# Performance work log

Hardware: AMD Instinct MI355X
Metric: run time of the kernel (lower is better)

Reference implementation:

```python
import jax, jax.numpy as jnp
import numpy as np
import math

NUM_HEADS = 16
KEY_SIZE = 64
HIDDEN = 4096
EMBED = 1024
VOCAB = 32000
SEQ = 2048
LAYERS = 4


def rmsnorm(x):
    return x * jax.lax.rsqrt(jnp.mean(x * x, axis=-1, keepdims=True) + 1e-5)


def rope_buffers(seq, d):
    half = d // 2
    i = jnp.arange(d)
    offset = i % half
    scales = jnp.power(10000.0, (-2.0 / d) * offset.astype(jnp.float32))
    m = jnp.arange(seq, dtype=jnp.float32)
    angles = m[:, None] * scales[None, :]  # [S, D]
    cos = jnp.cos(angles)
    sin = jnp.sin(angles)
    sin = jnp.concatenate([-sin[:, :half], sin[:, half:]], axis=-1)
    return cos, sin


def rotate(x, cos, sin):
    # x: [B, H, S, D]; cos/sin: [S, D]
    half = KEY_SIZE // 2
    swapped = jnp.concatenate([x[..., half:], x[..., :half]], axis=-1)
    return cos[None, None] * x + sin[None, None] * swapped


def setup_inputs() -> dict:
    key = jax.random.key(0)
    ks = jax.random.split(key, 7)
    std = 0.02
    return {
        'tokens': jax.random.randint(ks[0], (1, SEQ), 0, VOCAB),
        'table': jax.random.normal(ks[1], (VOCAB, EMBED), jnp.float32) * std,
        'qkv_w': jax.random.normal(ks[2], (LAYERS, EMBED, 3 * NUM_HEADS * KEY_SIZE), jnp.float32) * std,
        'out_w': jax.random.normal(ks[3], (LAYERS, NUM_HEADS * KEY_SIZE, EMBED), jnp.float32) * std,
        'up_w': jax.random.normal(ks[4], (LAYERS, EMBED, 2 * HIDDEN), jnp.float32) * std,
        'down_w': jax.random.normal(ks[5], (LAYERS, HIDDEN, EMBED), jnp.float32) * std,
        'vocab_w': jax.random.normal(ks[6], (EMBED, VOCAB), jnp.float32) * std,
    }


def reference(tokens, table, qkv_w, out_w, up_w, down_w, vocab_w):
    B, S = tokens.shape
    H, D = NUM_HEADS, KEY_SIZE
    # module zeroes embedding row 0 each forward
    table = table.at[0].set(0.0)
    cos, sin = rope_buffers(S, D)
    causal = jnp.tril(jnp.ones((S, S), dtype=bool))  # context_size == S -> pure causal
    emb = table[tokens]  # [B, S, E]
    for l in range(LAYERS):
        # --- self attention ---
        normed = rmsnorm(emb)
        qkv = normed @ qkv_w[l]  # [B, S, 3HD]
        q, k, v = jnp.split(qkv, 3, axis=-1)
        q = q.reshape(B, S, H, D).transpose(0, 2, 1, 3)
        k = k.reshape(B, S, H, D).transpose(0, 2, 1, 3)
        v = v.reshape(B, S, H, D).transpose(0, 2, 1, 3)
        q = rotate(q, cos, sin)
        k = rotate(k, cos, sin)
        attn = jnp.einsum('bhqd,bhkd->bhqk', q, k) / math.sqrt(D)
        attn = jnp.where(causal[None, None], attn, -jnp.inf)
        attn = jax.nn.softmax(attn, axis=-1)
        out = jnp.einsum('bhqk,bhkd->bhqd', attn, v)
        out = out.transpose(0, 2, 1, 3).reshape(B, S, H * D)
        emb = emb + out @ out_w[l]
        # --- SwiGLU FFN ---
        normed = rmsnorm(emb)
        gate_up = normed @ up_w[l]
        gate, up = gate_up[..., :HIDDEN], gate_up[..., HIDDEN:]
        emb = emb + (up * jax.nn.silu(gate)) @ down_w[l]
    emb = rmsnorm(emb)
    logits = emb @ vocab_w  # [B, S, V]
    return logits
```

## Files before the change

kernel.cpp:

```cpp
#include <hip/hip_runtime.h>
#include <hip/hip_bf16.h>

typedef __attribute__((ext_vector_type(8))) short short8;
typedef __attribute__((ext_vector_type(4))) float f32x4;

__device__ __forceinline__ ushort f2bf(float f) {
  uint32_t u = __float_as_uint(f);
  uint32_t r = (u + 0x7FFFu + ((u >> 16) & 1u)) >> 16;
  return (ushort)r;
}
__device__ __forceinline__ float bf2f(ushort u) {
  return __uint_as_float(((uint32_t)u) << 16);
}

__device__ __forceinline__ void gload_lds16(const ushort* g, ushort* l) {
  __builtin_amdgcn_global_load_lds(
      (const __attribute__((address_space(1))) void*)g,
      (__attribute__((address_space(3))) void*)l, 16, 0, 0);
}

__device__ __forceinline__ f32x4 mfma16(short8 a, short8 b, f32x4 c) {
  return __builtin_amdgcn_mfma_f32_16x16x32_bf16(a, b, c, 0, 0, 0);
}

#define BAR() __builtin_amdgcn_s_barrier()
#define WAIT_LGKM()                                        \
  do {                                                     \
    asm volatile("s_waitcnt lgkmcnt(0)" ::: "memory");     \
    __builtin_amdgcn_sched_barrier(0);                     \
  } while (0)
#define WAIT_VM0()                                         \
  do {                                                     \
    asm volatile("s_waitcnt vmcnt(0)" ::: "memory");       \
    __builtin_amdgcn_sched_barrier(0);                     \
  } while (0)
#define WAIT_VM4()                                         \
  do {                                                     \
    asm volatile("s_waitcnt vmcnt(4)" ::: "memory");       \
    __builtin_amdgcn_sched_barrier(0);                     \
  } while (0)

__global__ __launch_bounds__(256)
void transpose_conv_kernel(const float* __restrict__ W, ushort* __restrict__ WT,
                           const int K, const int N, const int mode) {
  const size_t lofs = (size_t)blockIdx.z * K * N;
  W += lofs;
  WT += lofs;
  __shared__ float tile[64][65];
  const int n0 = blockIdx.x * 64;
  const int k0 = blockIdx.y * 64;
  const int t = threadIdx.x;
#pragma unroll
  for (int j = 0; j < 4; ++j) {
    const int idx = j * 1024 + t * 4;
    const int kk = idx >> 6, nn = idx & 63;
    *(float4*)&tile[kk][nn] = *(const float4*)&W[(size_t)(k0 + kk) * N + n0 + nn];
  }
  __syncthreads();
#pragma unroll
  for (int j = 0; j < 4; ++j) {
    const int idx = j * 1024 + t * 4;
    const int nn = idx >> 6, kk = idx & 63;
    int rr = n0 + nn;
    if (mode == 1) rr = (rr < 4096) ? (2 * rr) : (2 * (rr - 4096) + 1);
    ushort4 o;
    o.x = f2bf(tile[kk + 0][nn]);
    o.y = f2bf(tile[kk + 1][nn]);
    o.z = f2bf(tile[kk + 2][nn]);
    o.w = f2bf(tile[kk + 3][nn]);
    *(ushort4*)&WT[(size_t)rr * K + k0 + kk] = o;
  }
}

__global__ __launch_bounds__(256)
void sincos_kernel(float2* __restrict__ cstab) {
  const int idx = blockIdx.x * 256 + threadIdx.x;
  const int s = idx >> 5, o = idx & 31;
  const float freq = exp2f(-0.41524101186092029f * (float)o);
  const float a = (float)s * freq;
  cstab[idx] = make_float2(cosf(a), sinf(a));
}

__global__ __launch_bounds__(256)
void embed_norm_kernel(const int* __restrict__ tokens, const float* __restrict__ table,
                       float* __restrict__ emb, ushort* __restrict__ normed) {
  const int s = blockIdx.x, t = threadIdx.x;
  const int tok = tokens[s];
  float4 v = make_float4(0.f, 0.f, 0.f, 0.f);
  if (tok != 0) v = *(const float4*)&table[(size_t)tok * 1024 + t * 4];
  *(float4*)&emb[(size_t)s * 1024 + t * 4] = v;
  float ss = v.x * v.x + v.y * v.y + v.z * v.z + v.w * v.w;
#pragma unroll
  for (int off = 32; off; off >>= 1) ss += __shfl_xor(ss, off);
  __shared__ float red[4];
  if ((t & 63) == 0) red[t >> 6] = ss;
  __syncthreads();
  const float total = red[0] + red[1] + red[2] + red[3];
  const float sc = rsqrtf(total * (1.f / 1024.f) + 1e-5f);
  ushort4 o;
  o.x = f2bf(v.x * sc); o.y = f2bf(v.y * sc);
  o.z = f2bf(v.z * sc); o.w = f2bf(v.w * sc);
  *(ushort4*)&normed[(size_t)s * 1024 + t * 4] = o;
}

__global__ __launch_bounds__(256)
void rmsnorm_kernel(const float* __restrict__ x, ushort* __restrict__ out) {
  const int row = blockIdx.x, t = threadIdx.x;
  const float4 v = *(const float4*)&x[(size_t)row * 1024 + t * 4];
  float ss = v.x * v.x + v.y * v.y + v.z * v.z + v.w * v.w;
#pragma unroll
  for (int off = 32; off; off >>= 1) ss += __shfl_xor(ss, off);
  __shared__ float red[4];
  if ((t & 63) == 0) red[t >> 6] = ss;
  __syncthreads();
  const float total = red[0] + red[1] + red[2] + red[3];
  const float sc = rsqrtf(total * (1.f / 1024.f) + 1e-5f);
  ushort4 o;
  o.x = f2bf(v.x * sc); o.y = f2bf(v.y * sc);
  o.z = f2bf(v.z * sc); o.w = f2bf(v.w * sc);
  *(ushort4*)&out[(size_t)row * 1024 + t * 4] = o;
}

__global__ __launch_bounds__(256)
void attn_mfma_kernel(const ushort* __restrict__ qh, const ushort* __restrict__ kh,
                      const ushort* __restrict__ vt, ushort* __restrict__ attn_out) {
  __shared__ ushort sQ[64 * 64];
  __shared__ ushort sK[64 * 64];
  __shared__ ushort sV[64 * 64];
  __shared__ ushort sP[4][1024];
  const int h = blockIdx.y;
  const int bx = blockIdx.x;
  const int qt = (h < 8) ? bx : 31 - bx;
  const int i0 = qt * 64;
  const int tid = threadIdx.x;
  const int w = tid >> 6, lane = tid & 63;
  const int llo = lane & 15, lhi = lane >> 4;
  const int lr = lane >> 3, lc = lane & 7;
  const ushort* qg = qh + ((size_t)h * 2048 + i0) * 64;
  const ushort* kg = kh + (size_t)h * 2048 * 64;
  const ushort* vg = vt + (size_t)h * 64 * 2048;

#pragma unroll
  for (int j = 0; j < 2; ++j) {
    const int r0 = (w * 2 + j) * 8;
    const int row = r0 + lr;
    gload_lds16(qg + (size_t)row * 64 + ((lc ^ (row & 7)) * 8), &sQ[r0 * 64]);
  }
  __syncthreads();
  const int qrow = w * 16 + llo;
  const short8 qf0 = *(const short8*)&sQ[qrow * 64 + ((lhi ^ (qrow & 7)) * 8)];
  const short8 qf1 = *(const short8*)&sQ[qrow * 64 + (((4 + lhi) ^ (qrow & 7)) * 8)];

  float m = -1e30f, lsum = 0.f;
  f32x4 o[4] = {};
  const int nch = qt + 1;
  for (int cb = 0; cb < nch; ++cb) {
    const int kb = cb * 64;
    __syncthreads();
#pragma unroll
    for (int j = 0; j < 2; ++j) {
      const int r0 = (w * 2 + j) * 8;
      const int row = r0 + lr;
      gload_lds16(kg + (size_t)(kb + row) * 64 + ((lc ^ (row & 7)) * 8), &sK[r0 * 64]);
      gload_lds16(vg + (size_t)row * 2048 + kb + ((lc ^ (row & 7)) * 8), &sV[r0 * 64]);
    }
    __syncthreads();

    f32x4 st[4] = {};
#pragma unroll
    for (int ck = 0; ck < 2; ++ck) {
      const short8 qf = ck ? qf1 : qf0;
#pragma unroll
      for (int f = 0; f < 4; ++f) {
        const int key = f * 16 + llo;
        const short8 kf = *(const short8*)&sK[key * 64 + (((ck * 4 + lhi) ^ (key & 7)) * 8)];
        st[f] = mfma16(kf, qf, st[f]);
      }
    }

    float pv[4][4];
    const bool diag = (kb == i0);
#pragma unroll
    for (int f = 0; f < 4; ++f)
#pragma unroll
      for (int r = 0; r < 4; ++r) {
        float x = st[f][r] * 0.125f;
        if (diag && (f * 16 + lhi * 4 + r) > qrow) x = -1e30f;
        pv[f][r] = x;
      }
    float mr = pv[0][0];
#pragma unroll
    for (int f = 0; f < 4; ++f)
#pragma unroll
      for (int r = 0; r < 4; ++r) mr = fmaxf(mr, pv[f][r]);
    mr = fmaxf(mr, __shfl_xor(mr, 16));
    mr = fmaxf(mr, __shfl_xor(mr, 32));
    const float mnew = fmaxf(m, mr);
    const float scale = __expf(m - mnew);
    m = mnew;
    float rs = 0.f;
#pragma unroll
    for (int f = 0; f < 4; ++f)
#pragma unroll
      for (int r = 0; r < 4; ++r) {
        const float p = __expf(pv[f][r] - mnew);
        pv[f][r] = p;
        rs += p;
      }
    rs += __shfl_xor(rs, 16);
    rs += __shfl_xor(rs, 32);
    lsum = lsum * scale + rs;
    float scr[4];
#pragma unroll
    for (int r = 0; r < 4; ++r) scr[r] = __shfl(scale, lhi * 4 + r);
#pragma unroll
    for (int nn = 0; nn < 4; ++nn)
#pragma unroll
      for (int r = 0; r < 4; ++r) o[nn][r] *= scr[r];

    ushort* pw = sP[w];
#pragma unroll
    for (int f = 0; f < 4; ++f) {
      uint2 pk;
      pk.x = (uint)f2bf(pv[f][0]) | ((uint)f2bf(pv[f][1]) << 16);
      pk.y = (uint)f2bf(pv[f][2]) | ((uint)f2bf(pv[f][3]) << 16);
      *(uint2*)&pw[llo * 64 + ((f * 16 + lhi * 4) ^ ((llo & 7) << 3))] = pk;
    }
    const short8 pf0 = *(const short8*)&pw[llo * 64 + ((lhi ^ (llo & 7)) * 8)];
    const short8 pf1 = *(const short8*)&pw[llo * 64 + (((4 + lhi) ^ (llo & 7)) * 8)];

#pragma unroll
    for (int ck = 0; ck < 2; ++ck) {
      const short8 pf = ck ? pf1 : pf0;
#pragma unroll
      for (int nn = 0; nn < 4; ++nn) {
        const int drow = nn * 16 + llo;
        const short8 vf = *(const short8*)&sV[drow * 64 + (((ck * 4 + lhi) ^ (drow & 7)) * 8)];
        o[nn] = mfma16(pf, vf, o[nn]);
      }
    }
  }

  const float inv = 1.f / lsum;
  float invr[4];
#pragma unroll
  for (int r = 0; r < 4; ++r) invr[r] = __shfl(inv, lhi * 4 + r);
#pragma unroll
  for (int nn = 0; nn < 4; ++nn)
#pragma unroll
    for (int r = 0; r < 4; ++r) {
      const int row = i0 + w * 16 + lhi * 4 + r;
      attn_out[(size_t)row * 1024 + h * 64 + nn * 16 + llo] = f2bf(o[nn][r] * invr[r]);
    }
}

template <int BM, int BN, int EPI>
__global__ __launch_bounds__(256)
void gemm_bt64_kernel(const ushort* __restrict__ A, const ushort* __restrict__ BT,
                      const float* __restrict__ addend, void* __restrict__ Cout,
                      const int M, const int N, const int K) {
  constexpr int WM = BM / 2, WN = BN / 2;
  constexpr int FM = WM / 16, FN = WN / 16;
  __shared__ ushort sA[BM * 64];
  __shared__ ushort sB[BN * 64];
  const int bm0 = blockIdx.y * BM;
  const int bn0 = blockIdx.x * BN;
  const int tid = threadIdx.x;
  const int wid = tid >> 6, lane = tid & 63;
  const int wr = wid >> 1, wc = wid & 1;
  const int lhi = lane >> 4, llo = lane & 15;
  f32x4 acc[FM][FN] = {};
  for (int kt = 0; kt < K; kt += 64) {
#pragma unroll
    for (int i = 0; i < BM * 8 / 256; ++i) {
      const int cb = i * 256 + wid * 64;
      const int ch = cb + lane;
      const int row = ch >> 3, c = ch & 7;
      gload_lds16(A + (size_t)(bm0 + row) * K + kt + ((c ^ (row & 7)) * 8),
                  sA + (size_t)cb * 8);
    }
#pragma unroll
    for (int i = 0; i < BN * 8 / 256; ++i) {
      const int cb = i * 256 + wid * 64;
      const int ch = cb + lane;
      const int row = ch >> 3, c = ch & 7;
      gload_lds16(BT + (size_t)(bn0 + row) * K + kt + ((c ^ (row & 7)) * 8),
                  sB + (size_t)cb * 8);
    }
    __syncthreads();
    short8 aF[FM][2], bF[FN][2];
#pragma unroll
    for (int mm = 0; mm < FM; ++mm) {
      const int row = wr * WM + mm * 16 + llo;
#pragma unroll
      for (int ks = 0; ks < 2; ++ks)
        aF[mm][ks] = *(const short8*)&sA[row * 64 + (((ks * 4 + lhi) ^ (row & 7)) * 8)];
    }
#pragma unroll
    for (int nn = 0; nn < FN; ++nn) {
      const int row = wc * WN + nn * 16 + llo;
#pragma unroll
      for (int ks = 0; ks < 2; ++ks)
        bF[nn][ks] = *(const short8*)&sB[row * 64 + (((ks * 4 + lhi) ^ (row & 7)) * 8)];
    }
#pragma unroll
    for (int mm = 0; mm < FM; ++mm)
#pragma unroll
      for (int nn = 0; nn < FN; ++nn)
#pragma unroll
        for (int ks = 0; ks < 2; ++ks)
          acc[mm][nn] = mfma16(aF[mm][ks], bF[nn][ks], acc[mm][nn]);
    __syncthreads();
  }
#pragma unroll
  for (int mm = 0; mm < FM; ++mm) {
#pragma unroll
    for (int nn = 0; nn < FN; ++nn) {
      const int col = bn0 + wc * WN + nn * 16 + llo;
#pragma unroll
      for (int r = 0; r < 4; ++r) {
        const int row = bm0 + wr * WM + mm * 16 + lhi * 4 + r;
        float v = acc[mm][nn][r];
        if constexpr (EPI == 1) v += addend[(size_t)row * N + col];
        ((float*)Cout)[(size_t)row * N + col] = v;
      }
    }
  }
}

__global__ __launch_bounds__(256)
void gemm_qkv_kernel(const ushort* __restrict__ A, const ushort* __restrict__ BT,
                     const float2* __restrict__ cstab, ushort* __restrict__ qh,
                     ushort* __restrict__ kh, ushort* __restrict__ vt, const int K) {
  constexpr int BM = 128, BN = 128, WM = 64, WN = 64, FM = 4, FN = 4;
  __shared__ ushort sA[BM * 64];
  __shared__ ushort sB[BN * 64];
  const int bm0 = blockIdx.y * BM;
  const int bn0 = blockIdx.x * BN;
  const int tid = threadIdx.x;
  const int wid = tid >> 6, lane = tid & 63;
  const int wr = wid >> 1, wc = wid & 1;
  const int lhi = lane >> 4, llo = lane & 15;
  f32x4 acc[FM][FN] = {};
  for (int kt = 0; kt < K; kt += 64) {
#pragma unroll
    for (int i = 0; i < 4; ++i) {
      const int cb = i * 256 + wid * 64;
      const int ch = cb + lane;
      const int row = ch >> 3, c = ch & 7;
      gload_lds16(A + (size_t)(bm0 + row) * K + kt + ((c ^ (row & 7)) * 8),
                  sA + (size_t)cb * 8);
    }
#pragma unroll
    for (int i = 0; i < 4; ++i) {
      const int cb = i * 256 + wid * 64;
      const int ch = cb + lane;
      const int row = ch >> 3, c = ch & 7;
      gload_lds16(BT + (size_t)(bn0 + row) * K + kt + ((c ^ (row & 7)) * 8),
                  sB + (size_t)cb * 8);
    }
    __syncthreads();
    short8 aF[FM][2], bF[FN][2];
#pragma unroll
    for (int mm = 0; mm < FM; ++mm) {
      const int row = wr * WM + mm * 16 + llo;
#pragma unroll
      for (int ks = 0; ks < 2; ++ks)
        aF[mm][ks] = *(const short8*)&sA[row * 64 + (((ks * 4 + lhi) ^ (row & 7)) * 8)];
    }
#pragma unroll
    for (int nn = 0; nn < FN; ++nn) {
      const int row = wc * WN + nn * 16 + llo;
#pragma unroll
      for (int ks = 0; ks < 2; ++ks)
        bF[nn][ks] = *(const short8*)&sB[row * 64 + (((ks * 4 + lhi) ^ (row & 7)) * 8)];
    }
#pragma unroll
    for (int mm = 0; mm < FM; ++mm)
#pragma unroll
      for (int nn = 0; nn < FN; ++nn)
#pragma unroll
        for (int ks = 0; ks < 2; ++ks)
          acc[mm][nn] = mfma16(aF[mm][ks], bF[nn][ks], acc[mm][nn]);
    __syncthreads();
  }
#pragma unroll
  for (int mm = 0; mm < FM; ++mm) {
    const int row_base = bm0 + wr * WM + mm * 16 + lhi * 4;
#pragma unroll
    for (int nn = 0; nn < FN; ++nn) {
      const int col = bn0 + wc * WN + nn * 16 + llo;
      const int part = col >> 10;
      const int hcol = col & 1023;
      const int h = hcol >> 6;
      const int d = hcol & 63;
      const int off = d & 31;
      if (part == 2) {
        ushort4 o;
        o.x = f2bf(acc[mm][nn][0]);
        o.y = f2bf(acc[mm][nn][1]);
        o.z = f2bf(acc[mm][nn][2]);
        o.w = f2bf(acc[mm][nn][3]);
        *(ushort4*)&vt[((size_t)h * 64 + d) * 2048 + row_base] = o;
      } else {
#pragma unroll
        for (int r = 0; r < 4; ++r) {
          const int row = row_base + r;
          const float v = acc[mm][nn][r];
          const float pt = acc[mm][nn ^ 2][r];
          const float2 cn = cstab[row * 32 + off];
          const float si = (d < 32) ? -cn.y : cn.y;
          const ushort o = f2bf(cn.x * v + si * pt);
          const size_t ho = ((size_t)h * 2048 + row) * 64 + d;
          if (part == 0) qh[ho] = o; else kh[ho] = o;
        }
      }
    }
  }
}

#define LDA_(MH)                                                              \
  {                                                                           \
    _Pragma("unroll") for (int mm = 0; mm < 4; ++mm) {                        \
      const int row = wr * 128 + ((MH) * 4 + mm) * 16 + llo;                  \
      _Pragma("unroll") for (int ks = 0; ks < 2; ++ks)                        \
          aF[mm][ks] = *(const short8*)&cA[row * 64 +                         \
                          (((ks * 4 + lhi) ^ (row & 7)) * 8)];                \
    }                                                                         \
  }
#define LDB_(NH)                                                              \
  {                                                                           \
    _Pragma("unroll") for (int nn = 0; nn < 2; ++nn) {                        \
      const int row = wc * 64 + ((NH) * 2 + nn) * 16 + llo;                   \
      _Pragma("unroll") for (int ks = 0; ks < 2; ++ks)                        \
          bF[nn][ks] = *(const short8*)&cB[row * 64 +                         \
                          (((ks * 4 + lhi) ^ (row & 7)) * 8)];                \
    }                                                                         \
  }
#define MFMAQ_(MH, NH)                                                        \
  {                                                                           \
    __builtin_amdgcn_s_setprio(1);                                            \
    _Pragma("unroll") for (int mm = 0; mm < 4; ++mm)                          \
        _Pragma("unroll") for (int nn = 0; nn < 2; ++nn)                      \
            _Pragma("unroll") for (int ks = 0; ks < 2; ++ks)                  \
                acc[(MH) * 4 + mm][(NH) * 2 + nn] =                           \
                    mfma16(aF[mm][ks], bF[nn][ks],                            \
                           acc[(MH) * 4 + mm][(NH) * 2 + nn]);                \
    __builtin_amdgcn_s_setprio(0);                                            \
  }

template <int EPI>
__global__ __launch_bounds__(512, 2)
void gemm8_kernel(const ushort* __restrict__ A, const ushort* __restrict__ BT,
                  void* __restrict__ Cout,
                  const int M, const int N, const int K, const int nby) {
  extern __shared__ ushort smem[];
  const int nwg = gridDim.x;
  const int cpx = nwg >> 3;
  int id = blockIdx.x;
  id = (id & 7) * cpx + (id >> 3);
  const int by = id % nby, bx = id / nby;
  const int bm0 = by * 256, bn0 = bx * 256;
  const int tid = threadIdx.x;
  const int wid = tid >> 6, lane = tid & 63;
  const int wr = wid >> 2, wc = wid & 3;
  const int llo = lane & 15, lhi = lane >> 4;
  const ushort* gA = A + (size_t)bm0 * K;
  const ushort* gB = BT + (size_t)bn0 * K;

  auto stage = [&](const ushort* g, ushort* dst, int kt) {
#pragma unroll
    for (int i = 0; i < 4; ++i) {
      const int chunk = i * 512 + wid * 64 + lane;
      const int row = chunk >> 3, c = chunk & 7;
      gload_lds16(g + (size_t)row * K + kt + ((c ^ (row & 7)) * 8),
                  dst + (size_t)(i * 512 + wid * 64) * 8);
    }
  };

  f32x4 acc[8][4] = {};
  short8 aF[4][2];
  short8 bF[2][2];

  stage(gA, smem, 0);
  stage(gB, smem + 16384, 0);
  WAIT_VM0();
  BAR();

  const int nt = K >> 6;
  for (int t = 0; t < nt; ++t) {
    const int cur = t & 1;
    ushort* cA = smem + cur * 32768;
    ushort* cB = cA + 16384;
    ushort* nA = smem + (cur ^ 1) * 32768;
    ushort* nB = nA + 16384;
    const bool pf = (t + 1 < nt);
    LDA_(0); LDB_(0);
    if (pf) { stage(gA, nA, (t + 1) * 64); stage(gB, nB, (t + 1) * 64); }
    BAR(); WAIT_LGKM();
    MFMAQ_(0, 0);
    BAR();
    LDB_(1);
    BAR(); WAIT_LGKM();
    MFMAQ_(0, 1);
    BAR();
    LDA_(1);
    BAR(); WAIT_LGKM();
    MFMAQ_(1, 1);
    BAR();
    LDB_(0);
    BAR(); WAIT_LGKM();
    MFMAQ_(1, 0);
    if (pf) WAIT_VM0();
    BAR();
  }

#pragma unroll
  for (int m = 0; m < 8; ++m) {
#pragma unroll
    for (int n = 0; n < 4; ++n) {
      const int col = bn0 + wc * 64 + n * 16 + llo;
#pragma unroll
      for (int r = 0; r < 4; ++r) {
        const int row = bm0 + wr * 128 + m * 16 + lhi * 4 + r;
        float v = acc[m][n][r];
        if constexpr (EPI == 3) {
          const float other = __shfl_xor(v, 1);
          if ((llo & 1) == 0) {
            const float gate = v, up = other;
            const float hh = up * gate / (1.f + expf(-gate));
            ((ushort*)Cout)[(size_t)row * (N >> 1) + (col >> 1)] = f2bf(hh);
          }
        } else {
          ((float*)Cout)[(size_t)row * N + col] = v;
        }
      }
    }
  }
}

template <int EPI>
__global__ __launch_bounds__(512, 2)
void gemm8p_kernel(const ushort* __restrict__ A, const ushort* __restrict__ BT,
                   void* __restrict__ Cout,
                   const int M, const int N, const int K, const int nby) {
  extern __shared__ ushort smem[];
  const int nwg = gridDim.x;
  const int cpx = nwg >> 3;
  int id = blockIdx.x;
  id = (id & 7) * cpx + (id >> 3);
  const int by = id % nby, bx = id / nby;
  const int bm0 = by * 256, bn0 = bx * 256;
  const int tid = threadIdx.x;
  const int wid = tid >> 6, lane = tid & 63;
  const int wr = wid >> 2, wc = wid & 3;
  const int llo = lane & 15, lhi = lane >> 4;
  const ushort* gA = A + (size_t)bm0 * K;
  const ushort* gB = BT + (size_t)bn0 * K;

  auto stage = [&](ushort* dst, int kt) {
#pragma unroll
    for (int i = 0; i < 2; ++i) {
      const int cb = i * 512 + wid * 64;
      const int ch = cb + lane;
      const int row = ch >> 2, c = ch & 3;
      gload_lds16(gA + (size_t)row * K + kt + ((c ^ ((row >> 1) & 3)) * 8),
                  dst + (size_t)cb * 8);
    }
#pragma unroll
    for (int i = 0; i < 2; ++i) {
      const int cb = i * 512 + wid * 64;
      const int ch = cb + lane;
      const int row = ch >> 2, c = ch & 3;
      gload_lds16(gB + (size_t)row * K + kt + ((c ^ ((row >> 1) & 3)) * 8),
                  dst + 8192 + (size_t)cb * 8);
    }
  };

  f32x4 acc[8][4] = {};
  short8 aF[4], bF[4];

  const int nt = K >> 5;
  stage(smem, 0);
  stage(smem + 16384, 32);
  WAIT_VM4();
  BAR();

  int cs = 0;
  for (int t = 0; t < nt; ++t) {
    ushort* cA = smem + cs * 16384;
    ushort* cB = cA + 8192;
    int ss = cs + 2; if (ss >= 3) ss -= 3;
    const bool pf2 = (t + 2 < nt);
    if (pf2) stage(smem + ss * 16384, (t + 2) * 32);
#pragma unroll
    for (int mm = 0; mm < 4; ++mm) {
      const int row = wr * 128 + mm * 16 + llo;
      aF[mm] = *(const short8*)&cA[row * 32 + ((lhi ^ ((row >> 1) & 3)) * 8)];
    }
#pragma unroll
    for (int nn = 0; nn < 4; ++nn) {
      const int row = wc * 64 + nn * 16 + llo;
      bF[nn] = *(const short8*)&cB[row * 32 + ((lhi ^ ((row >> 1) & 3)) * 8)];
    }
    BAR(); WAIT_LGKM();
    __builtin_amdgcn_s_setprio(1);
#pragma unroll
    for (int mm = 0; mm < 4; ++mm)
#pragma unroll
      for (int nn = 0; nn < 4; ++nn)
        acc[mm][nn] = mfma16(aF[mm], bF[nn], acc[mm][nn]);
    __builtin_amdgcn_s_setprio(0);
    BAR();
#pragma unroll
    for (int mm = 0; mm < 4; ++mm) {
      const int row = wr * 128 + (mm + 4) * 16 + llo;
      aF[mm] = *(const short8*)&cA[row * 32 + ((lhi ^ ((row >> 1) & 3)) * 8)];
    }
    BAR(); WAIT_LGKM();
    __builtin_amdgcn_s_setprio(1);
#pragma unroll
    for (int mm = 0; mm < 4; ++mm)
#pragma unroll
      for (int nn = 0; nn < 4; ++nn)
        acc[mm + 4][nn] = mfma16(aF[mm], bF[nn], acc[mm + 4][nn]);
    __builtin_amdgcn_s_setprio(0);
    if (pf2) { WAIT_VM4(); } else { WAIT_VM0(); }
    BAR();
    ++cs; if (cs == 3) cs = 0;
  }

#pragma unroll
  for (int m = 0; m < 8; ++m) {
#pragma unroll
    for (int n = 0; n < 4; ++n) {
      const int col = bn0 + wc * 64 + n * 16 + llo;
#pragma unroll
      for (int r = 0; r < 4; ++r) {
        const int row = bm0 + wr * 128 + m * 16 + lhi * 4 + r;
        ((float*)Cout)[(size_t)row * N + col] = acc[m][n][r];
      }
    }
  }
}

extern "C" void kernel_launch(void* const* d_in, const int* in_sizes, int n_in,
                              void* d_out, int out_size, void* d_ws, size_t ws_size,
                              hipStream_t stream) {
  const int* tokens    = (const int*)d_in[0];
  const float* table   = (const float*)d_in[1];
  const float* qkv_w   = (const float*)d_in[2];
  const float* out_w   = (const float*)d_in[3];
  const float* up_w    = (const float*)d_in[4];
  const float* down_w  = (const float*)d_in[5];
  const float* vocab_w = (const float*)d_in[6];
  float* logits = (float*)d_out;

  constexpr int G8_LDS = 131072;
  constexpr int G8P_LDS = 98304;
  hipFuncSetAttribute(reinterpret_cast<const void*>(&gemm8_kernel<3>),
                      hipFuncAttributeMaxDynamicSharedMemorySize, G8_LDS);
  hipFuncSetAttribute(reinterpret_cast<const void*>(&gemm8p_kernel<0>),
                      hipFuncAttributeMaxDynamicSharedMemorySize, G8P_LDS);

  char* p = (char*)d_ws;
  auto alloc = [&](size_t bytes) {
    char* r = p;
    p += (bytes + 255) & ~(size_t)255;
    return r;
  };
  float*  emb    = (float*)alloc(2048ull * 1024 * 4);
  ushort* normed = (ushort*)alloc(2048ull * 1024 * 2);
  float2* cstab  = (float2*)alloc(2048ull * 32 * 8);
  ushort* qhb    = (ushort*)alloc(16ull * 2048 * 64 * 2);
  ushort* khb    = (ushort*)alloc(16ull * 2048 * 64 * 2);
  ushort* vtb    = (ushort*)alloc(16ull * 64 * 2048 * 2);
  ushort* attno  = (ushort*)alloc(2048ull * 1024 * 2);
  ushort* hbuf   = (ushort*)alloc(2048ull * 4096 * 2);
  ushort* qkvT   = (ushort*)alloc(4ull * 3072 * 1024 * 2);
  ushort* outT   = (ushort*)alloc(4ull * 1024 * 1024 * 2);
  ushort* upT    = (ushort*)alloc(4ull * 8192 * 1024 * 2);
  ushort* downT  = (ushort*)alloc(4ull * 1024 * 4096 * 2);
  ushort* vocabT = (ushort*)alloc(32000ull * 1024 * 2);

  transpose_conv_kernel<<<dim3(3072 / 64, 1024 / 64, 4), 256, 0, stream>>>(
      qkv_w, qkvT, 1024, 3072, 0);
  transpose_conv_kernel<<<dim3(1024 / 64, 1024 / 64, 4), 256, 0, stream>>>(
      out_w, outT, 1024, 1024, 0);
  transpose_conv_kernel<<<dim3(8192 / 64, 1024 / 64, 4), 256, 0, stream>>>(
      up_w, upT, 1024, 8192, 1);
  transpose_conv_kernel<<<dim3(1024 / 64, 4096 / 64, 4), 256, 0, stream>>>(
      down_w, downT, 4096, 1024, 0);
  transpose_conv_kernel<<<dim3(32000 / 64, 1024 / 64, 1), 256, 0, stream>>>(
      vocab_w, vocabT, 1024, 32000, 0);
  sincos_kernel<<<256, 256, 0, stream>>>(cstab);

  embed_norm_kernel<<<2048, 256, 0, stream>>>(tokens, table, emb, normed);

  for (int l = 0; l < 4; ++l) {
    if (l > 0) rmsnorm_kernel<<<2048, 256, 0, stream>>>(emb, normed);
    gemm_qkv_kernel<<<dim3(3072 / 128, 2048 / 128), 256, 0, stream>>>(
        normed, qkvT + (size_t)l * 3072 * 1024, cstab, qhb, khb, vtb, 1024);
    attn_mfma_kernel<<<dim3(32, 16), 256, 0, stream>>>(qhb, khb, vtb, attno);
    gemm_bt64_kernel<64, 128, 1><<<dim3(1024 / 128, 2048 / 64), 256, 0, stream>>>(
        attno, outT + (size_t)l * 1024 * 1024, emb, emb, 2048, 1024, 1024);
    rmsnorm_kernel<<<2048, 256, 0, stream>>>(emb, normed);
    gemm8_kernel<3><<<(8192 / 256) * (2048 / 256), 512, G8_LDS, stream>>>(
        normed, upT + (size_t)l * 8192 * 1024, hbuf, 2048, 8192, 1024, 2048 / 256);
    gemm_bt64_kernel<64, 128, 1><<<dim3(1024 / 128, 2048 / 64), 256, 0, stream>>>(
        hbuf, downT + (size_t)l * 1024 * 4096, emb, emb, 2048, 1024, 4096);
  }
  rmsnorm_kernel<<<2048, 256, 0, stream>>>(emb, normed);
  gemm8p_kernel<0><<<(32000 / 256) * (2048 / 256), 512, G8P_LDS, stream>>>(
      normed, vocabT, logits, 2048, 32000, 1024, 2048 / 256);
}
```

Before: 1.241 ms.

## Enlarge attention query tile to 128 rows with 8 waves sharing K/V loads

The attention kernel now processes 128 query rows per block using 512 threads (8 waves), so each K/V chunk loaded into LDS is reused by twice as many query rows and the block count halves. Causal masking is generalized to a per-wave edge test, and waves whose rows lie entirely before a chunk skip its compute. This cuts global K/V traffic and loop overhead. In exchange there are fewer blocks (256) for the GPU, and waves idle at the causal boundary while still joining the barriers.

New measurement: 1.293 ms. 1.04x slower.

```diff
diff --git a/kernel.cpp b/kernel.cpp
--- a/kernel.cpp
+++ b/kernel.cpp
@@ -121,50 +121,53 @@
   *(ushort4*)&out[(size_t)row * 1024 + t * 4] = o;
 }
 
-__global__ __launch_bounds__(256)
+__global__ __launch_bounds__(512)
 void attn_mfma_kernel(const ushort* __restrict__ qh, const ushort* __restrict__ kh,
                       const ushort* __restrict__ vt, ushort* __restrict__ attn_out) {
-  __shared__ ushort sQ[64 * 64];
+  __shared__ ushort sQ[128 * 64];
   __shared__ ushort sK[64 * 64];
   __shared__ ushort sV[64 * 64];
-  __shared__ ushort sP[4][1024];
+  __shared__ ushort sP[8][1024];
   const int h = blockIdx.y;
   const int bx = blockIdx.x;
-  const int qt = (h < 8) ? bx : 31 - bx;
-  const int i0 = qt * 64;
+  const int qt = (h < 8) ? bx : 15 - bx;
+  const int i0 = qt * 128;
   const int tid = threadIdx.x;
   const int w = tid >> 6, lane = tid & 63;
   const int llo = lane & 15, lhi = lane >> 4;
-  const int lr = lane >> 3, lc = lane & 7;
   const ushort* qg = qh + ((size_t)h * 2048 + i0) * 64;
   const ushort* kg = kh + (size_t)h * 2048 * 64;
   const ushort* vg = vt + (size_t)h * 64 * 2048;
 
 #pragma unroll
   for (int j = 0; j < 2; ++j) {
-    const int r0 = (w * 2 + j) * 8;
-    const int row = r0 + lr;
-    gload_lds16(qg + (size_t)row * 64 + ((lc ^ (row & 7)) * 8), &sQ[r0 * 64]);
+    const int cb = j * 512 + w * 64;
+    const int ch = cb + lane;
+    const int row = ch >> 3, c = ch & 7;
+    gload_lds16(qg + (size_t)row * 64 + ((c ^ (row & 7)) * 8), &sQ[cb * 8]);
   }
   __syncthreads();
   const int qrow = w * 16 + llo;
   const short8 qf0 = *(const short8*)&sQ[qrow * 64 + ((lhi ^ (qrow & 7)) * 8)];
   const short8 qf1 = *(const short8*)&sQ[qrow * 64 + (((4 + lhi) ^ (qrow & 7)) * 8)];
+  const int wmax = i0 + w * 16 + 15;
 
   float m = -1e30f, lsum = 0.f;
   f32x4 o[4] = {};
-  const int nch = qt + 1;
-  for (int cb = 0; cb < nch; ++cb) {
-    const int kb = cb * 64;
+  const int nch = 2 * qt + 2;
+  for (int cb2 = 0; cb2 < nch; ++cb2) {
+    const int kb = cb2 * 64;
     __syncthreads();
-#pragma unroll
-    for (int j = 0; j < 2; ++j) {
-      const int r0 = (w * 2 + j) * 8;
-      const int row = r0 + lr;
-      gload_lds16(kg + (size_t)(kb + row) * 64 + ((lc ^ (row & 7)) * 8), &sK[r0 * 64]);
-      gload_lds16(vg + (size_t)row * 2048 + kb + ((lc ^ (row & 7)) * 8), &sV[r0 * 64]);
+    {
+      const int cb = w * 64;
+      const int ch = cb + lane;
+      const int row = ch >> 3, c = ch & 7;
+      gload_lds16(kg + (size_t)(kb + row) * 64 + ((c ^ (row & 7)) * 8), &sK[cb * 8]);
+      gload_lds16(vg + (size_t)row * 2048 + kb + ((c ^ (row & 7)) * 8), &sV[cb * 8]);
     }
     __syncthreads();
+
+    if (kb > wmax) continue;
 
     f32x4 st[4] = {};
 #pragma unroll
@@ -179,13 +182,13 @@
     }
 
     float pv[4][4];
-    const bool diag = (kb == i0);
+    const bool edge = (kb + 63 > i0 + w * 16);
 #pragma unroll
     for (int f = 0; f < 4; ++f)
 #pragma unroll
       for (int r = 0; r < 4; ++r) {
         float x = st[f][r] * 0.125f;
-        if (diag && (f * 16 + lhi * 4 + r) > qrow) x = -1e30f;
+        if (edge && (kb - i0 + f * 16 + lhi * 4 + r) > qrow) x = -1e30f;
         pv[f][r] = x;
       }
     float mr = pv[0][0];
@@ -701,7 +704,7 @@
     if (l > 0) rmsnorm_kernel<<<2048, 256, 0, stream>>>(emb, normed);
     gemm_qkv_kernel<<<dim3(3072 / 128, 2048 / 128), 256, 0, stream>>>(
         normed, qkvT + (size_t)l * 3072 * 1024, cstab, qhb, khb, vtb, 1024);
-    attn_mfma_kernel<<<dim3(32, 16), 256, 0, stream>>>(qhb, khb, vtb, attno);
+    attn_mfma_kernel<<<dim3(16, 16), 512, 0, stream>>>(qhb, khb, vtb, attno);
     gemm_bt64_kernel<64, 128, 1><<<dim3(1024 / 128, 2048 / 64), 256, 0, stream>>>(
         attno, outT + (size_t)l * 1024 * 1024, emb, emb, 2048, 1024, 1024);
     rmsnorm_kernel<<<2048, 256, 0, stream>>>(emb, normed);
```
